# Kernel optimization log

Hardware: AMD Instinct MI355X
Metric: run time of the kernel (lower is better)

## Reference

```python
import jax, jax.numpy as jnp
import numpy as np

B, L, E, H = 64, 256, 1024, 16
HD = E // H
ROPE_BASE = 10000.0


def rope(x):
    # x: [B, H, L, HD]; torchtune-style interleaved RoPE along the seq axis
    Lx, D = x.shape[2], x.shape[3]
    inv_freq = 1.0 / (ROPE_BASE ** (jnp.arange(0, D, 2, dtype=jnp.float32) / D))
    ang = jnp.arange(Lx, dtype=jnp.float32)[:, None] * inv_freq[None, :]  # [L, D/2]
    cos, sin = jnp.cos(ang), jnp.sin(ang)
    x0, x1 = x[..., 0::2], x[..., 1::2]
    r0 = x0 * cos - x1 * sin
    r1 = x1 * cos + x0 * sin
    return jnp.stack([r0, r1], axis=-1).reshape(x.shape)


def setup_inputs() -> dict:
    key = jax.random.key(0)
    ks = jax.random.split(key, 6)
    s = 0.02
    return {
        "x": jax.random.normal(ks[0], (B, L, E), jnp.float32),
        "Wq": jax.random.normal(ks[1], (E, E), jnp.float32) * s,
        "bq": jnp.zeros((E,), jnp.float32),
        "Wk": jax.random.normal(ks[2], (E, E), jnp.float32) * s,
        "bk": jnp.zeros((E,), jnp.float32),
        "Wv": jax.random.normal(ks[3], (E, E), jnp.float32) * s,
        "bv": jnp.zeros((E,), jnp.float32),
        "Wo": jax.random.normal(ks[4], (E, E), jnp.float32) * s,
        "bo": jnp.zeros((E,), jnp.float32),
        "attention_mask": jnp.ones((B, L), bool),
    }


def reference(x, Wq, bq, Wk, bk, Wv, bv, Wo, bo, attention_mask):
    Bq, Lq, _ = x.shape
    # QKV projections (nn.Linear: y = x @ W.T + b), split heads -> [B, H, L, HD]
    q = (x @ Wq.T + bq).reshape(Bq, Lq, H, HD).transpose(0, 2, 1, 3)
    k = (x @ Wk.T + bk).reshape(Bq, Lq, H, HD).transpose(0, 2, 1, 3)
    v = (x @ Wv.T + bv).reshape(Bq, Lq, H, HD).transpose(0, 2, 1, 3)
    q = rope(q)
    k = rope(k)
    # combined causal + padding mask: [B, 1, Lq, Lq]
    causal = jnp.tril(jnp.ones((Lq, Lq), bool))
    mask = causal[None, None, :, :] & attention_mask[:, None, None, :]
    scale = 1.0 / np.sqrt(HD).astype(np.float32)
    scores = jnp.einsum('bhqd,bhkd->bhqk', q, k) * scale
    scores = jnp.where(mask, scores, jnp.finfo(scores.dtype).min)
    attn = jax.nn.softmax(scores, axis=-1)
    out = jnp.einsum('bhqk,bhkd->bhqd', attn, v)
    out = out.transpose(0, 2, 1, 3).reshape(Bq, Lq, E)
    return out @ Wo.T + bo
```

## Files before the change

kernel.cpp:

```cpp
#include <hip/hip_runtime.h>
#include <hip/hip_bf16.h>

typedef __attribute__((ext_vector_type(4))) float f32x4;
typedef __attribute__((ext_vector_type(8))) short s16x8;
typedef unsigned short ushort_t;

__device__ __forceinline__ ushort_t f2bf(float f) {
    union { float f; unsigned u; } v; v.f = f;
    unsigned r = v.u + 0x7fffu + ((v.u >> 16) & 1u);
    return (ushort_t)(r >> 16);
}

__device__ __forceinline__ void gload16(const ushort_t* g, ushort_t* l) {
    __builtin_amdgcn_global_load_lds(
        (const __attribute__((address_space(1))) unsigned int*)g,
        (__attribute__((address_space(3))) unsigned int*)l,
        16, 0, 0);
}

#define BAR()  asm volatile("s_barrier" ::: "memory")
#define LGK0() do { asm volatile("s_waitcnt lgkmcnt(0)" ::: "memory"); __builtin_amdgcn_sched_barrier(0); } while (0)
#define VMC(n) asm volatile("s_waitcnt vmcnt(" #n ")" ::: "memory")

__global__ void cvt_bf16(const float* __restrict__ in, ushort_t* __restrict__ out, int n8) {
    int i = blockIdx.x * blockDim.x + threadIdx.x;
    if (i >= n8) return;
    const float4* p = (const float4*)in;
    float4 a = p[2 * i], b = p[2 * i + 1];
    s16x8 v;
    v[0] = (short)f2bf(a.x); v[1] = (short)f2bf(a.y);
    v[2] = (short)f2bf(a.z); v[3] = (short)f2bf(a.w);
    v[4] = (short)f2bf(b.x); v[5] = (short)f2bf(b.y);
    v[6] = (short)f2bf(b.z); v[7] = (short)f2bf(b.w);
    *(s16x8*)(out + (size_t)i * 8) = v;
}

__global__ void rope_tab_k(float* __restrict__ cosT, float* __restrict__ sinT) {
    int i = blockIdx.x * blockDim.x + threadIdx.x;
    int l = i >> 5, fi = i & 31;
    float inv = powf(10000.f, -2.f * (float)fi / 64.f);
    float ang = (float)l * inv;
    cosT[i] = cosf(ang);
    sinT[i] = sinf(ang);
}


__device__ __forceinline__ void stage_half(const ushort_t* __restrict__ src,
                                           ushort_t* chunk, int tid) {
#pragma unroll
    for (int j = 0; j < 2; ++j) {
        int row = (tid >> 3) + j * 64;
        int gslot = (tid & 7) ^ (row & 7);
        gload16(src + (size_t)row * 1024 + gslot * 8,
                chunk + (size_t)tid * 8 + (size_t)j * 4096);
    }
}

__device__ __forceinline__ s16x8 rdA(const ushort_t* chunk, int m, int kh, int lane) {
    int row = m * 16 + (lane & 15);
    int slot = (kh * 4 + (lane >> 4)) ^ (row & 7);
    return *(const s16x8*)&chunk[row * 64 + (slot << 3)];
}
__device__ __forceinline__ s16x8 rdB(const ushort_t* chunk, int wn, int n, int kh, int lane) {
    int row = (wn & 1) * 64 + n * 16 + (lane & 15);
    int slot = (kh * 4 + (lane >> 4)) ^ (row & 7);
    return *(const s16x8*)&chunk[row * 64 + (slot << 3)];
}

#define MFMA_Q(q, x, y)                                                                              \
    do {                                                                                             \
        _Pragma("unroll") for (int n_ = 0; n_ < 4; ++n_) {                                           \
            acc[2*(q)][n_]   = __builtin_amdgcn_mfma_f32_16x16x32_bf16(x[0], b_[n_][0], acc[2*(q)][n_], 0, 0, 0);   \
            acc[2*(q)][n_]   = __builtin_amdgcn_mfma_f32_16x16x32_bf16(x[1], b_[n_][1], acc[2*(q)][n_], 0, 0, 0);   \
            acc[2*(q)+1][n_] = __builtin_amdgcn_mfma_f32_16x16x32_bf16(y[0], b_[n_][0], acc[2*(q)+1][n_], 0, 0, 0); \
            acc[2*(q)+1][n_] = __builtin_amdgcn_mfma_f32_16x16x32_bf16(y[1], b_[n_][1], acc[2*(q)+1][n_], 0, 0, 0); \
        }                                                                                            \
    } while (0)

template <int MODE>
__global__ __launch_bounds__(512, 2) void gemm256(const ushort_t* __restrict__ A,
                                                  const ushort_t* __restrict__ Wt,
                                                  const float* __restrict__ bz0,
                                                  const float* __restrict__ bz1,
                                                  const float* __restrict__ bz2,
                                                  ushort_t* __restrict__ o0,
                                                  ushort_t* __restrict__ o1,
                                                  ushort_t* __restrict__ o2,
                                                  float* __restrict__ of,
                                                  const float* __restrict__ cosT,
                                                  const float* __restrict__ sinT,
                                                  int ntn) {
    __shared__ ushort_t lds[2][4][8192];
#define Lc(b, c) (&lds[b][c][0])

    const int nwg = 64 * ntn;
    const int orig = blockIdx.x;
    const int wg = (orig % 8) * (nwg / 8) + orig / 8;
    const int tn = wg % ntn, tm = wg / ntn;

    const int tid = threadIdx.x, lane = tid & 63, wid = tid >> 6;
    const int wm = wid >> 2, wn = wid & 3;

    f32x4 acc[8][4];
#pragma unroll
    for (int i = 0; i < 8; ++i)
#pragma unroll
        for (int j = 0; j < 4; ++j) acc[i][j] = (f32x4){0.f, 0.f, 0.f, 0.f};

    const ushort_t* Abase = A + (size_t)(tm * 256) * 1024;
    const ushort_t* Bbase = Wt + (size_t)(tn * 256) * 1024;

    stage_half(Bbase, Lc(0, 2), tid);
    stage_half(Bbase + (size_t)128 * 1024, Lc(0, 3), tid);
    stage_half(Abase, Lc(0, 0), tid);
    stage_half(Abase + (size_t)128 * 1024, Lc(0, 1), tid);
    VMC(0);
    BAR();
    stage_half(Bbase + 64, Lc(1, 2), tid);
    stage_half(Bbase + (size_t)128 * 1024 + 64, Lc(1, 3), tid);
    stage_half(Abase + 64, Lc(1, 0), tid);

#pragma unroll 1
    for (int u = 0; u < 16; ++u) {
        const int bu = u & 1;
        const ushort_t* cA = Lc(bu, wm);
        const ushort_t* cB = Lc(bu, 2 + (wn >> 1));
        const int kk1 = (u + 1 < 16 ? u + 1 : 15) * 64;
        const int kk2 = (u + 2 < 16 ? u + 2 : 15) * 64;
        s16x8 b_[4][2], a0[2], a1[2], a2[2], a3[2], a4[2], a5[2], a6[2], a7[2];

        VMC(6);
#pragma unroll
        for (int n = 0; n < 4; ++n)
#pragma unroll
            for (int kh = 0; kh < 2; ++kh) b_[n][kh] = rdB(cB, wn, n, kh, lane);
#pragma unroll
        for (int kh = 0; kh < 2; ++kh) { a0[kh] = rdA(cA, 0, kh, lane); a1[kh] = rdA(cA, 1, kh, lane); }
        stage_half(Abase + (size_t)128 * 1024 + kk1, Lc((u + 1) & 1, 1), tid);
        BAR(); LGK0();
        __builtin_amdgcn_s_setprio(1);
        MFMA_Q(0, a0, a1);
        __builtin_amdgcn_s_setprio(0);
        BAR();

#pragma unroll
        for (int kh = 0; kh < 2; ++kh) {
            a2[kh] = rdA(cA, 2, kh, lane); a3[kh] = rdA(cA, 3, kh, lane);
            a4[kh] = rdA(cA, 4, kh, lane); a5[kh] = rdA(cA, 5, kh, lane);
        }
        stage_half(Bbase + kk2, Lc(bu, 2), tid);
        BAR(); LGK0();
        __builtin_amdgcn_s_setprio(1);
        MFMA_Q(1, a2, a3);
        __builtin_amdgcn_s_setprio(0);
        BAR();

#pragma unroll
        for (int kh = 0; kh < 2; ++kh) { a6[kh] = rdA(cA, 6, kh, lane); a7[kh] = rdA(cA, 7, kh, lane); }
        stage_half(Bbase + (size_t)128 * 1024 + kk2, Lc(bu, 3), tid);
        BAR(); LGK0();
        __builtin_amdgcn_s_setprio(1);
        MFMA_Q(2, a4, a5);
        __builtin_amdgcn_s_setprio(0);
        BAR();

        stage_half(Abase + kk2, Lc(bu, 0), tid);
        BAR(); LGK0();
        __builtin_amdgcn_s_setprio(1);
        MFMA_Q(3, a6, a7);
        __builtin_amdgcn_s_setprio(0);
        BAR();
    }
    VMC(0);

    const int rb0 = tm * 256 + wm * 128 + ((lane >> 4) << 2);
    if (MODE == 0) {
        const int zz = (tn * 256) >> 10;
        const float* bias = (zz == 0) ? bz0 : (zz == 1) ? bz1 : bz2;
        ushort_t* outp = (zz == 0) ? o0 : (zz == 1) ? o1 : o2;
        const bool rope = (zz < 2);
        const int cb = (tn & 3) * 256 + wn * 64;
#pragma unroll
        for (int m = 0; m < 8; ++m) {
#pragma unroll
            for (int n = 0; n < 4; ++n) {
                int col = cb + n * 16 + (lane & 15);
                float bv_ = bias[col];
                int rb = rb0 + m * 16;
#pragma unroll
                for (int r = 0; r < 4; ++r) {
                    float v = acc[m][n][r] + bv_;
                    float res;
                    if (rope) {
                        int l = (rb + r) & 255;
                        int fi = (col & 63) >> 1;
                        float c = cosT[l * 32 + fi], s = sinT[l * 32 + fi];
                        float partner = __shfl_xor(v, 1);
                        res = (col & 1) ? (v * c + partner * s) : (v * c - partner * s);
                    } else {
                        res = v;
                    }
                    outp[(size_t)(rb + r) * 1024 + col] = f2bf(res);
                }
            }
        }
    } else {
        const int cb = wn * 64;
        const int cfull = tn * 256 + cb;
#pragma unroll
        for (int m = 0; m < 8; ++m) {
#pragma unroll
            for (int n = 0; n < 4; ++n) {
                int col = cfull + n * 16 + (lane & 15);
                float bv_ = bz0[col];
                int rb = rb0 + m * 16;
#pragma unroll
                for (int r = 0; r < 4; ++r)
                    of[(size_t)(rb + r) * 1024 + col] = acc[m][n][r] + bv_;
            }
        }
    }
#undef Lc
}

__global__ __launch_bounds__(512) void attn_kernel(const ushort_t* __restrict__ qb,
                                                   const ushort_t* __restrict__ kb,
                                                   const ushort_t* __restrict__ vb,
                                                   ushort_t* __restrict__ ab) {
    __shared__ ushort_t Ks[256 * 72];
    __shared__ ushort_t Vt[64 * 264];
    __shared__ ushort_t Ps[8][16 * 264];
    const int bh = blockIdx.x, b = bh >> 4, h = bh & 15;
    const int tid = threadIdx.x, lane = tid & 63, wid = tid >> 6;
    const size_t base = (size_t)b * 256 * 1024 + (size_t)h * 64;

#pragma unroll
    for (int it = 0; it < 4; ++it) {
        int c = tid + it * 512;
        int row = c >> 3, seg = c & 7;
        *(s16x8*)&Ks[row * 72 + seg * 8] =
            *(const s16x8*)&kb[base + (size_t)row * 1024 + seg * 8];
    }
#pragma unroll
    for (int it = 0; it < 4; ++it) {
        int c = tid + it * 512;
        int k = c >> 3, seg = c & 7;
        s16x8 v8 = *(const s16x8*)&vb[base + (size_t)k * 1024 + seg * 8];
#pragma unroll
        for (int j = 0; j < 8; ++j)
            Vt[(seg * 8 + j) * 264 + k] = (ushort_t)v8[j];
    }
    __syncthreads();

#pragma unroll
    for (int ch = 0; ch < 2; ++ch) {
        const int q0 = wid * 32 + ch * 16;
        const int ntop = q0 >> 4;
        s16x8 aq0 = *(const s16x8*)&qb[base + (size_t)(q0 + (lane & 15)) * 1024 + ((lane >> 4) << 3)];
        s16x8 aq1 = *(const s16x8*)&qb[base + (size_t)(q0 + (lane & 15)) * 1024 + 32 + ((lane >> 4) << 3)];

        f32x4 sacc[16];
#pragma unroll
        for (int n = 0; n < 16; ++n) sacc[n] = (f32x4){0.f, 0.f, 0.f, 0.f};
#pragma unroll
        for (int n = 0; n < 16; ++n) {
            if (n <= ntop) {
                const int kr = (n * 16 + (lane & 15)) * 72 + ((lane >> 4) << 3);
                s16x8 b0 = *(const s16x8*)&Ks[kr];
                s16x8 b1 = *(const s16x8*)&Ks[kr + 32];
                sacc[n] = __builtin_amdgcn_mfma_f32_16x16x32_bf16(aq0, b0, sacc[n], 0, 0, 0);
                sacc[n] = __builtin_amdgcn_mfma_f32_16x16x32_bf16(aq1, b1, sacc[n], 0, 0, 0);
            }
        }

        float rinv[4];
#pragma unroll
        for (int r = 0; r < 4; ++r) {
            const int row = q0 + ((lane >> 4) << 2) + r;
            float m = -1e30f;
#pragma unroll
            for (int n = 0; n < 16; ++n) {
                int col = n * 16 + (lane & 15);
                float v = (col <= row) ? sacc[n][r] * 0.125f : -1e30f;
                sacc[n][r] = v;
                m = fmaxf(m, v);
            }
            m = fmaxf(m, __shfl_xor(m, 1));
            m = fmaxf(m, __shfl_xor(m, 2));
            m = fmaxf(m, __shfl_xor(m, 4));
            m = fmaxf(m, __shfl_xor(m, 8));
            float sum = 0.f;
#pragma unroll
            for (int n = 0; n < 16; ++n) {
                float p = __expf(sacc[n][r] - m);
                sacc[n][r] = p;
                sum += p;
            }
            sum += __shfl_xor(sum, 1);
            sum += __shfl_xor(sum, 2);
            sum += __shfl_xor(sum, 4);
            sum += __shfl_xor(sum, 8);
            rinv[r] = 1.f / sum;
#pragma unroll
            for (int n = 0; n < 16; ++n)
                Ps[wid][(((lane >> 4) << 2) + r) * 264 + n * 16 + (lane & 15)] = f2bf(sacc[n][r]);
        }
        __syncthreads();

        f32x4 oa[4];
#pragma unroll
        for (int dt = 0; dt < 4; ++dt) oa[dt] = (f32x4){0.f, 0.f, 0.f, 0.f};
        const int kstop = q0 >> 5;
#pragma unroll
        for (int ks = 0; ks < 8; ++ks) {
            if (ks <= kstop) {
                s16x8 pf = *(const s16x8*)&Ps[wid][(lane & 15) * 264 + ks * 32 + ((lane >> 4) << 3)];
#pragma unroll
                for (int dt = 0; dt < 4; ++dt) {
                    s16x8 vf = *(const s16x8*)&Vt[(dt * 16 + (lane & 15)) * 264 + ks * 32 + ((lane >> 4) << 3)];
                    oa[dt] = __builtin_amdgcn_mfma_f32_16x16x32_bf16(pf, vf, oa[dt], 0, 0, 0);
                }
            }
        }
#pragma unroll
        for (int dt = 0; dt < 4; ++dt) {
#pragma unroll
            for (int r = 0; r < 4; ++r) {
                int row = q0 + ((lane >> 4) << 2) + r;
                int col = h * 64 + dt * 16 + (lane & 15);
                ab[(size_t)(b * 256 + row) * 1024 + col] = f2bf(oa[dt][r] * rinv[r]);
            }
        }
        __syncthreads();
    }
}

extern "C" void kernel_launch(void* const* d_in, const int* in_sizes, int n_in,
                              void* d_out, int out_size, void* d_ws, size_t ws_size,
                              hipStream_t stream) {
    (void)in_sizes; (void)n_in; (void)out_size;
    const float* x  = (const float*)d_in[0];
    const float* Wq = (const float*)d_in[1];
    const float* bq = (const float*)d_in[2];
    const float* Wk = (const float*)d_in[3];
    const float* bk = (const float*)d_in[4];
    const float* Wv = (const float*)d_in[5];
    const float* bv = (const float*)d_in[6];
    const float* Wo = (const float*)d_in[7];
    const float* bo = (const float*)d_in[8];
    float* out = (float*)d_out;

    const size_t M = 16384, E = 1024;
    char* ws = (char*)d_ws;
    ushort_t* xb   = (ushort_t*)ws;
    ushort_t* wqkv = xb + M * E;
    ushort_t* wob  = wqkv + 3 * E * E;
    ushort_t* qb   = wob + E * E;
    ushort_t* kb   = qb + M * E;
    ushort_t* vb   = kb + M * E;
    float* cosT    = (float*)(vb + M * E);
    float* sinT    = cosT + 256 * 32;
    ushort_t* ab   = xb;

    size_t need = (4 * M * E + 4 * E * E) * sizeof(ushort_t) + 2 * 256 * 32 * sizeof(float);
    if (ws_size < need) return;

    cvt_bf16<<<8192, 256, 0, stream>>>(x, xb, (int)(M * E / 8));
    cvt_bf16<<<512, 256, 0, stream>>>(Wq, wqkv, (int)(E * E / 8));
    cvt_bf16<<<512, 256, 0, stream>>>(Wk, wqkv + E * E, (int)(E * E / 8));
    cvt_bf16<<<512, 256, 0, stream>>>(Wv, wqkv + 2 * E * E, (int)(E * E / 8));
    cvt_bf16<<<512, 256, 0, stream>>>(Wo, wob, (int)(E * E / 8));
    rope_tab_k<<<32, 256, 0, stream>>>(cosT, sinT);

    gemm256<0><<<768, 512, 0, stream>>>(xb, wqkv, bq, bk, bv, qb, kb, vb, nullptr,
                                        cosT, sinT, 12);
    attn_kernel<<<1024, 512, 0, stream>>>(qb, kb, vb, ab);
    gemm256<1><<<256, 512, 0, stream>>>(ab, wob, bo, nullptr, nullptr,
                                        nullptr, nullptr, nullptr, out, nullptr, nullptr, 4);
}
```

Baseline: 282.8 us.

## Restructure GEMM main loop to 4-stage K=32 LDS ring buffer

Replaces the double-buffered K=64 tile pipeline with a four-slot ring of K=32 stages, prefetching three stages ahead. Each iteration now does two MFMA phases instead of four, with fewer barriers per K step and deeper prefetch. Swizzle and read helpers are adapted to 32-wide rows. The cost is twice as many loop iterations and narrower LDS rows, which may change bank-conflict and barrier behaviour.

After: 297.6 us. 5.2% more time.

```diff
diff --git a/kernel.cpp b/kernel.cpp
--- a/kernel.cpp
+++ b/kernel.cpp
@@ -45,37 +45,27 @@
 }
 
 
-__device__ __forceinline__ void stage_half(const ushort_t* __restrict__ src,
-                                           ushort_t* chunk, int tid) {
+__device__ __forceinline__ void stage32(const ushort_t* __restrict__ src,
+                                        ushort_t* chunk, int tid, int kk) {
 #pragma unroll
     for (int j = 0; j < 2; ++j) {
-        int row = (tid >> 3) + j * 64;
-        int gslot = (tid & 7) ^ (row & 7);
-        gload16(src + (size_t)row * 1024 + gslot * 8,
+        int row = (tid >> 2) + j * 128;
+        int gslot = (tid & 3) ^ (row & 3);
+        gload16(src + (size_t)row * 1024 + kk + gslot * 8,
                 chunk + (size_t)tid * 8 + (size_t)j * 4096);
     }
 }
 
-__device__ __forceinline__ s16x8 rdA(const ushort_t* chunk, int m, int kh, int lane) {
-    int row = m * 16 + (lane & 15);
-    int slot = (kh * 4 + (lane >> 4)) ^ (row & 7);
-    return *(const s16x8*)&chunk[row * 64 + (slot << 3)];
-}
-__device__ __forceinline__ s16x8 rdB(const ushort_t* chunk, int wn, int n, int kh, int lane) {
-    int row = (wn & 1) * 64 + n * 16 + (lane & 15);
-    int slot = (kh * 4 + (lane >> 4)) ^ (row & 7);
-    return *(const s16x8*)&chunk[row * 64 + (slot << 3)];
-}
-
-#define MFMA_Q(q, x, y)                                                                              \
-    do {                                                                                             \
-        _Pragma("unroll") for (int n_ = 0; n_ < 4; ++n_) {                                           \
-            acc[2*(q)][n_]   = __builtin_amdgcn_mfma_f32_16x16x32_bf16(x[0], b_[n_][0], acc[2*(q)][n_], 0, 0, 0);   \
-            acc[2*(q)][n_]   = __builtin_amdgcn_mfma_f32_16x16x32_bf16(x[1], b_[n_][1], acc[2*(q)][n_], 0, 0, 0);   \
-            acc[2*(q)+1][n_] = __builtin_amdgcn_mfma_f32_16x16x32_bf16(y[0], b_[n_][0], acc[2*(q)+1][n_], 0, 0, 0); \
-            acc[2*(q)+1][n_] = __builtin_amdgcn_mfma_f32_16x16x32_bf16(y[1], b_[n_][1], acc[2*(q)+1][n_], 0, 0, 0); \
-        }                                                                                            \
-    } while (0)
+__device__ __forceinline__ s16x8 rdA32(const ushort_t* chunk, int wm, int m, int lane) {
+    int row = wm * 128 + m * 16 + (lane & 15);
+    int slot = (lane >> 4) ^ (row & 3);
+    return *(const s16x8*)&chunk[row * 32 + (slot << 3)];
+}
+__device__ __forceinline__ s16x8 rdB32(const ushort_t* chunk, int wn, int n, int lane) {
+    int row = wn * 64 + n * 16 + (lane & 15);
+    int slot = (lane >> 4) ^ (row & 3);
+    return *(const s16x8*)&chunk[row * 32 + (slot << 3)];
+}
 
 template <int MODE>
 __global__ __launch_bounds__(512, 2) void gemm256(const ushort_t* __restrict__ A,
@@ -90,8 +80,7 @@
                                                   const float* __restrict__ cosT,
                                                   const float* __restrict__ sinT,
                                                   int ntn) {
-    __shared__ ushort_t lds[2][4][8192];
-#define Lc(b, c) (&lds[b][c][0])
+    __shared__ ushort_t lds[4][2][8192];
 
     const int nwg = 64 * ntn;
     const int orig = blockIdx.x;
@@ -110,64 +99,49 @@
     const ushort_t* Abase = A + (size_t)(tm * 256) * 1024;
     const ushort_t* Bbase = Wt + (size_t)(tn * 256) * 1024;
 
-    stage_half(Bbase, Lc(0, 2), tid);
-    stage_half(Bbase + (size_t)128 * 1024, Lc(0, 3), tid);
-    stage_half(Abase, Lc(0, 0), tid);
-    stage_half(Abase + (size_t)128 * 1024, Lc(0, 1), tid);
-    VMC(0);
+#pragma unroll
+    for (int p = 0; p < 3; ++p) {
+        stage32(Abase, &lds[p][0][0], tid, p * 32);
+        stage32(Bbase, &lds[p][1][0], tid, p * 32);
+    }
+    VMC(8);
     BAR();
-    stage_half(Bbase + 64, Lc(1, 2), tid);
-    stage_half(Bbase + (size_t)128 * 1024 + 64, Lc(1, 3), tid);
-    stage_half(Abase + 64, Lc(1, 0), tid);
 
 #pragma unroll 1
-    for (int u = 0; u < 16; ++u) {
-        const int bu = u & 1;
-        const ushort_t* cA = Lc(bu, wm);
-        const ushort_t* cB = Lc(bu, 2 + (wn >> 1));
-        const int kk1 = (u + 1 < 16 ? u + 1 : 15) * 64;
-        const int kk2 = (u + 2 < 16 ? u + 2 : 15) * 64;
-        s16x8 b_[4][2], a0[2], a1[2], a2[2], a3[2], a4[2], a5[2], a6[2], a7[2];
-
-        VMC(6);
-#pragma unroll
-        for (int n = 0; n < 4; ++n)
-#pragma unroll
-            for (int kh = 0; kh < 2; ++kh) b_[n][kh] = rdB(cB, wn, n, kh, lane);
-#pragma unroll
-        for (int kh = 0; kh < 2; ++kh) { a0[kh] = rdA(cA, 0, kh, lane); a1[kh] = rdA(cA, 1, kh, lane); }
-        stage_half(Abase + (size_t)128 * 1024 + kk1, Lc((u + 1) & 1, 1), tid);
+    for (int u = 0; u < 32; ++u) {
+        const ushort_t* cA = &lds[u & 3][0][0];
+        const ushort_t* cB = &lds[u & 3][1][0];
+        ushort_t* sA = &lds[(u + 3) & 3][0][0];
+        ushort_t* sB = &lds[(u + 3) & 3][1][0];
+        const int kt = (u + 3 < 32 ? u + 3 : 31) * 32;
+        s16x8 b_[4], a_[4], a2_[4];
+
+#pragma unroll
+        for (int n = 0; n < 4; ++n) b_[n] = rdB32(cB, wn, n, lane);
+#pragma unroll
+        for (int m = 0; m < 4; ++m) a_[m] = rdA32(cA, wm, m, lane);
+        stage32(Abase, sA, tid, kt);
         BAR(); LGK0();
         __builtin_amdgcn_s_setprio(1);
-        MFMA_Q(0, a0, a1);
+#pragma unroll
+        for (int m = 0; m < 4; ++m)
+#pragma unroll
+            for (int n = 0; n < 4; ++n)
+                acc[m][n] = __builtin_amdgcn_mfma_f32_16x16x32_bf16(a_[m], b_[n], acc[m][n], 0, 0, 0);
         __builtin_amdgcn_s_setprio(0);
         BAR();
 
 #pragma unroll
-        for (int kh = 0; kh < 2; ++kh) {
-            a2[kh] = rdA(cA, 2, kh, lane); a3[kh] = rdA(cA, 3, kh, lane);
-            a4[kh] = rdA(cA, 4, kh, lane); a5[kh] = rdA(cA, 5, kh, lane);
-        }
-        stage_half(Bbase + kk2, Lc(bu, 2), tid);
+        for (int m = 0; m < 4; ++m) a2_[m] = rdA32(cA, wm, m + 4, lane);
+        stage32(Bbase, sB, tid, kt);
+        VMC(8);
         BAR(); LGK0();
         __builtin_amdgcn_s_setprio(1);
-        MFMA_Q(1, a2, a3);
-        __builtin_amdgcn_s_setprio(0);
-        BAR();
-
-#pragma unroll
-        for (int kh = 0; kh < 2; ++kh) { a6[kh] = rdA(cA, 6, kh, lane); a7[kh] = rdA(cA, 7, kh, lane); }
-        stage_half(Bbase + (size_t)128 * 1024 + kk2, Lc(bu, 3), tid);
-        BAR(); LGK0();
-        __builtin_amdgcn_s_setprio(1);
-        MFMA_Q(2, a4, a5);
-        __builtin_amdgcn_s_setprio(0);
-        BAR();
-
-        stage_half(Abase + kk2, Lc(bu, 0), tid);
-        BAR(); LGK0();
-        __builtin_amdgcn_s_setprio(1);
-        MFMA_Q(3, a6, a7);
+#pragma unroll
+        for (int m = 0; m < 4; ++m)
+#pragma unroll
+            for (int n = 0; n < 4; ++n)
+                acc[m + 4][n] = __builtin_amdgcn_mfma_f32_16x16x32_bf16(a2_[m], b_[n], acc[m + 4][n], 0, 0, 0);
         __builtin_amdgcn_s_setprio(0);
         BAR();
     }
@@ -220,7 +194,6 @@
             }
         }
     }
-#undef Lc
 }
 
 __global__ __launch_bounds__(512) void attn_kernel(const ushort_t* __restrict__ qb,
```
